# Kernel optimization log

Hardware: AMD Instinct MI355X
Metric: run time of the kernel (lower is better)

Reference implementation:

```python
import jax, jax.numpy as jnp
import numpy as np

BATCH = 4096
DIM = 2048
TEMPERATURE = 0.5


def setup_inputs() -> dict:
    key = jax.random.key(0)
    k1, k2 = jax.random.split(key)
    c_i = jax.random.normal(k1, (BATCH, DIM), dtype=jnp.float32)
    c_j = jax.random.normal(k2, (BATCH, DIM), dtype=jnp.float32)
    return {"c_i": c_i, "c_j": c_j}


def reference(c_i, c_j):
    # Original torch loop computes, for each i,j:
    #   kl[i, j] = sum_k softmax(c_j[j])_k * (log_softmax(c_j[j])_k - log_softmax(c_i[i])_k)
    #   logits = -kl / T ; loss = CE(logits, arange(B), reduction='sum') / B
    # Fused: kl = hneg[None, :] - Li @ Q.T where hneg[j] = sum_k Q[j]*logQ[j].
    B = c_i.shape[0]
    Li = jax.nn.log_softmax(c_i, axis=-1)          # [B, D]
    LQ = jax.nn.log_softmax(c_j, axis=-1)          # [B, D]
    Q = jnp.exp(LQ)                                # softmax(c_j)
    hneg = jnp.sum(Q * LQ, axis=-1)                # [B] negative entropy of each c_j row
    cross = jnp.einsum("id,jd->ij", Li, Q)         # [B, B] sum_k Li[i,k]*Q[j,k]
    kl = hneg[None, :] - cross                     # [B, B]
    logits = -kl / TEMPERATURE
    logp = jax.nn.log_softmax(logits, axis=-1)     # [B, B]
    loss = -jnp.sum(jnp.diagonal(logp)) / B        # CE(sum) / batch_size
    return loss
```

## Files before the change

### kernel.cpp

```cpp
#include <hip/hip_runtime.h>
#include <hip/hip_bf16.h>
#include <math.h>

#define BATCH 4096
#define DIM   2048
#define INV_T 2.0f

#define BM 256
#define BN 256

typedef float floatx4 __attribute__((ext_vector_type(4)));
typedef int   intx4   __attribute__((ext_vector_type(4)));
typedef int   intx8   __attribute__((ext_vector_type(8)));

static __device__ __forceinline__ void gld_lds16(const void* g, void* l) {
  __builtin_amdgcn_global_load_lds(
      (const __attribute__((address_space(1))) void*)g,
      (__attribute__((address_space(3))) void*)l, 16, 0, 0);
}

static __device__ __forceinline__ intx8 comb8(intx4 lo, intx4 hi) {
  intx8 r;
  r[0] = lo[0]; r[1] = lo[1]; r[2] = lo[2]; r[3] = lo[3];
  r[4] = hi[0]; r[5] = hi[1]; r[6] = hi[2]; r[7] = hi[3];
  return r;
}

__global__ __launch_bounds__(256) void prep_kernel(
    const float* __restrict__ ci, const float* __restrict__ cj,
    unsigned char* __restrict__ Li8, unsigned char* __restrict__ Qb8,
    float* __restrict__ hneg, float* __restrict__ isc,
    float* __restrict__ rowsum, float* __restrict__ out)
{
  const int lane = threadIdx.x & 63;
  const int wave = threadIdx.x >> 6;
  const int row = blockIdx.x * 4 + wave;
  const bool isj = row >= BATCH;
  const int r = isj ? row - BATCH : row;
  const float* __restrict__ src = (isj ? cj : ci) + (size_t)r * DIM;

  float v[32];
  #pragma unroll
  for (int i = 0; i < 8; ++i) {
    float4 t = ((const float4*)src)[i * 64 + lane];
    v[i * 4 + 0] = t.x; v[i * 4 + 1] = t.y;
    v[i * 4 + 2] = t.z; v[i * 4 + 3] = t.w;
  }

  float m = v[0];
  #pragma unroll
  for (int i = 1; i < 32; ++i) m = fmaxf(m, v[i]);
  #pragma unroll
  for (int off = 32; off >= 1; off >>= 1) m = fmaxf(m, __shfl_xor(m, off));

  float s = 0.f;
  #pragma unroll
  for (int i = 0; i < 32; ++i) s += __expf(v[i] - m);
  #pragma unroll
  for (int off = 32; off >= 1; off >>= 1) s += __shfl_xor(s, off);
  const float ls = m + __logf(s);

  float scale = 1.f;
  int t = 0;
  if (isj) {
    const float qmax = __expf(m - ls);
    const int be = (int)((__float_as_uint(qmax) >> 23) & 0xff);
    t = 134 - be;
    scale = __uint_as_float((unsigned)(t + 127) << 23);
  }

  unsigned char* dst = (isj ? Qb8 : Li8) + (size_t)r * DIM;
  float h = 0.f;
  #pragma unroll
  for (int i = 0; i < 8; ++i) {
    float f[4];
    #pragma unroll
    for (int j = 0; j < 4; ++j) {
      const float li = v[i * 4 + j] - ls;
      if (isj) {
        const float q = __expf(li);
        h += q * li;
        f[j] = q * scale;
      } else {
        f[j] = li;
      }
    }
    int w = __builtin_amdgcn_cvt_pk_fp8_f32(f[0], f[1], 0, false);
    w = __builtin_amdgcn_cvt_pk_fp8_f32(f[2], f[3], w, true);
    if (isj) {
      const int idx = ((r >> 4) << 13) | ((i * 2 + (lane >> 5)) << 9)
                    | (((lane >> 3) & 3) << 7) | ((r & 15) << 3) | (lane & 7);
      ((int*)Qb8)[idx] = w;
    } else {
      ((int*)dst)[i * 64 + lane] = w;
    }
  }

  if (isj) {
    #pragma unroll
    for (int off = 32; off >= 1; off >>= 1) h += __shfl_xor(h, off);
    if (lane == 0) {
      hneg[r] = h;
      isc[r] = __uint_as_float((unsigned)(127 - t) << 23);
      rowsum[r] = 0.f;
    }
  }
  if (row == 0 && lane == 0) out[0] = 0.f;
}

__global__ __launch_bounds__(512, 1) void gemm_lse_kernel(
    const unsigned char* __restrict__ Li8, const unsigned char* __restrict__ Qb8,
    const float* __restrict__ hneg, const float* __restrict__ isc,
    float* __restrict__ rowsum, float* __restrict__ diag)
{
  __shared__ __attribute__((aligned(16))) unsigned char As_[2][BM * 128];

  const int tid  = threadIdx.x;
  const int lin = blockIdx.x;
  const int xc  = lin & 7;
  const int sq  = lin >> 3;
  const int by  = (xc & 3) * 4 + (sq & 3);
  const int bx  = (xc >> 2) * 8 + (sq >> 2);

  const int lane = tid & 63;
  const int wave = tid >> 6;
  const int wm   = wave >> 2;
  const int wn   = wave & 3;

  int soff[4];
  #pragma unroll
  for (int s = 0; s < 4; ++s) {
    const int p = tid + 512 * s;
    const int row = p >> 3;
    const int cbg = (p & 7) ^ (row & 7);
    soff[s] = row * DIM + cbg * 16;
  }
  const unsigned char* Abase = Li8 + (size_t)(by * BM) * DIM;
  const unsigned char* Bfbase =
      Qb8 + (size_t)(bx * 16 + wn * 4) * 32768 + lane * 32;

  const int rl = lane & 15;
  const int q  = lane >> 4;
  const int sw = rl & 7;

  floatx4 acc[8][4];
  const floatx4 z = {0.f, 0.f, 0.f, 0.f};
  #pragma unroll
  for (int mt = 0; mt < 8; ++mt)
    #pragma unroll
    for (int nt = 0; nt < 4; ++nt) acc[mt][nt] = z;

  #pragma unroll
  for (int s = 0; s < 4; ++s)
    gld_lds16(Abase + soff[s], &As_[0][0] + (tid + 512 * s) * 16);
  intx8 bfA[4], bfB[4];
  #pragma unroll
  for (int nt = 0; nt < 4; ++nt)
    bfA[nt] = comb8(*(const intx4*)(Bfbase + nt * 32768),
                    *(const intx4*)(Bfbase + nt * 32768 + 16));

#define KTILE(T, CUR, bfU, bfN)                                               \
  {                                                                           \
    const int t_ = (T);                                                       \
    const unsigned char* Ab = &As_[CUR][0];                                   \
    if (t_ < 15) {                                                            \
      unsigned char* An = &As_[(CUR) ^ 1][0];                                 \
      const int kn = (t_ + 1) * 128;                                          \
      _Pragma("unroll")                                                       \
      for (int s = 0; s < 4; ++s)                                             \
        gld_lds16(Abase + soff[s] + kn, An + (tid + 512 * s) * 16);           \
      _Pragma("unroll")                                                       \
      for (int nt = 0; nt < 4; ++nt)                                          \
        bfN[nt] = comb8(                                                      \
            *(const intx4*)(Bfbase + nt * 32768 + (t_ + 1) * 2048),           \
            *(const intx4*)(Bfbase + nt * 32768 + (t_ + 1) * 2048 + 16));     \
      asm volatile("s_waitcnt vmcnt(12)" ::: "memory");                       \
    } else {                                                                  \
      asm volatile("s_waitcnt vmcnt(0)" ::: "memory");                        \
    }                                                                         \
    asm volatile("s_barrier" ::: "memory");                                   \
    intx8 af[2];                                                              \
    {                                                                         \
      const int ra = wm * 128 + rl;                                           \
      const int a0 = ra * 8 + ((2 * q) ^ sw);                                 \
      const int a1 = ra * 8 + ((2 * q + 1) ^ sw);                             \
      af[0] = comb8(*(const intx4*)(Ab + a0 * 16),                            \
                    *(const intx4*)(Ab + a1 * 16));                           \
    }                                                                         \
    _Pragma("unroll")                                                         \
    for (int s = 0; s < 8; ++s) {                                             \
      if (s < 7) {                                                            \
        const int ra = wm * 128 + (s + 1) * 16 + rl;                          \
        const int a0 = ra * 8 + ((2 * q) ^ sw);                               \
        const int a1 = ra * 8 + ((2 * q + 1) ^ sw);                           \
        af[(s + 1) & 1] = comb8(*(const intx4*)(Ab + a0 * 16),                \
                                *(const intx4*)(Ab + a1 * 16));               \
      }                                                                       \
      __builtin_amdgcn_s_setprio(1);                                          \
      _Pragma("unroll")                                                       \
      for (int nt = 0; nt < 4; ++nt)                                          \
        acc[s][nt] = __builtin_amdgcn_mfma_scale_f32_16x16x128_f8f6f4(        \
            af[s & 1], bfU[nt], acc[s][nt],                                   \
            0, 0,                     \
            0, 127,                                         \
            0, 127);                                        \
      __builtin_amdgcn_s_setprio(0);                                          \
    }                                                                         \
    asm volatile("s_barrier" ::: "memory");                                   \
  }

  for (int tt = 0; tt < 8; ++tt) {
    KTILE(2 * tt,     0, bfA, bfB);
    KTILE(2 * tt + 1, 1, bfB, bfA);
  }
#undef KTILE

  const int col0 = bx * BN + wn * 64 + rl;
  float hn[4], sc[4];
  #pragma unroll
  for (int nt = 0; nt < 4; ++nt) {
    hn[nt] = hneg[col0 + nt * 16];
    sc[nt] = isc[col0 + nt * 16];
  }
  const int row0 = by * BM + wm * 128 + (q << 2);

  if (bx == by && wm == (wn >> 1) && q == (rl >> 2)) {
    #pragma unroll
    for (int half = 0; half < 2; ++half) {
      #pragma unroll
      for (int nt = 0; nt < 4; ++nt) {
        #pragma unroll
        for (int rr = 0; rr < 4; ++rr) {
          if ((wn & 1) == half && (rl & 3) == rr)
            diag[bx * BN + wn * 64 + nt * 16 + rl] =
                acc[half * 4 + nt][nt][rr] * sc[nt];
        }
      }
    }
  }

  #pragma unroll
  for (int mt = 0; mt < 8; ++mt) {
    #pragma unroll
    for (int rr = 0; rr < 4; ++rr) {
      float p = 0.f;
      #pragma unroll
      for (int nt = 0; nt < 4; ++nt)
        p += __expf(INV_T * (acc[mt][nt][rr] * sc[nt] - hn[nt]));
      p += __shfl_xor(p, 1);
      p += __shfl_xor(p, 2);
      p += __shfl_xor(p, 4);
      p += __shfl_xor(p, 8);
      if (rl == 0)
        atomicAdd(&rowsum[row0 + mt * 16 + rr], p);
    }
  }
}

__global__ __launch_bounds__(256) void finalize_kernel(
    const float* __restrict__ hneg, const float* __restrict__ rowsum,
    const float* __restrict__ diag, float* __restrict__ out)
{
  const int i = blockIdx.x * 256 + threadIdx.x;
  const int lane = threadIdx.x & 63;
  const int wave = threadIdx.x >> 6;

  float c = __logf(rowsum[i]) - INV_T * (diag[i] - hneg[i]);
  #pragma unroll
  for (int off = 32; off >= 1; off >>= 1) c += __shfl_xor(c, off);

  __shared__ float red[4];
  if (lane == 0) red[wave] = c;
  __syncthreads();
  if (threadIdx.x == 0)
    atomicAdd(out, (red[0] + red[1] + red[2] + red[3]) * (1.0f / BATCH));
}

extern "C" void kernel_launch(void* const* d_in, const int* in_sizes, int n_in,
                              void* d_out, int out_size, void* d_ws, size_t ws_size,
                              hipStream_t stream) {
  const float* ci = (const float*)d_in[0];
  const float* cj = (const float*)d_in[1];
  float* out = (float*)d_out;

  unsigned char* Li8 = (unsigned char*)d_ws;
  unsigned char* Qb8 = Li8 + (size_t)BATCH * DIM;
  float* hneg   = (float*)(Qb8 + (size_t)BATCH * DIM);
  float* isc    = hneg + BATCH;
  float* rowsum = isc + BATCH;
  float* diag   = rowsum + BATCH;

  prep_kernel<<<2 * BATCH / 4, 256, 0, stream>>>(ci, cj, Li8, Qb8, hneg, isc, rowsum, out);
  gemm_lse_kernel<<<(BATCH / BM) * (BATCH / BN), 512, 0, stream>>>(Li8, Qb8, hneg, isc, rowsum, diag);
  finalize_kernel<<<BATCH / 256, 256, 0, stream>>>(hneg, rowsum, diag, out);
}
```

Before: 166.6 us.

## Triple-buffer LDS A tiles with single barrier and reuse exp in prep

The GEMM main loop moves from double-buffered to triple-buffered LDS for the A operand. A tiles are prefetched two steps ahead, and each k-tile uses a single barrier instead of two. B fragments no longer ping-pong between two register sets: they are loaded into one set after each tile's MFMAs, which frees registers but may expose B load latency at the start of the next tile. The prep kernel also keeps the exponentials from the sum pass and builds softmax values by multiplying with a reciprocal, which drops a second exp per element.

```diff
diff --git a/kernel.cpp b/kernel.cpp
--- a/kernel.cpp
+++ b/kernel.cpp
@@ -53,23 +53,24 @@
   #pragma unroll
   for (int off = 32; off >= 1; off >>= 1) m = fmaxf(m, __shfl_xor(m, off));
 
+  float e[32];
   float s = 0.f;
   #pragma unroll
-  for (int i = 0; i < 32; ++i) s += __expf(v[i] - m);
+  for (int i = 0; i < 32; ++i) { e[i] = __expf(v[i] - m); s += e[i]; }
   #pragma unroll
   for (int off = 32; off >= 1; off >>= 1) s += __shfl_xor(s, off);
   const float ls = m + __logf(s);
+  const float inv_s = 1.0f / s;
 
   float scale = 1.f;
   int t = 0;
   if (isj) {
-    const float qmax = __expf(m - ls);
-    const int be = (int)((__float_as_uint(qmax) >> 23) & 0xff);
+    const int be = (int)((__float_as_uint(inv_s) >> 23) & 0xff);
     t = 134 - be;
     scale = __uint_as_float((unsigned)(t + 127) << 23);
   }
 
-  unsigned char* dst = (isj ? Qb8 : Li8) + (size_t)r * DIM;
+  unsigned char* dst = Li8 + (size_t)r * DIM;
   float h = 0.f;
   #pragma unroll
   for (int i = 0; i < 8; ++i) {
@@ -78,7 +79,7 @@
     for (int j = 0; j < 4; ++j) {
       const float li = v[i * 4 + j] - ls;
       if (isj) {
-        const float q = __expf(li);
+        const float q = e[i * 4 + j] * inv_s;
         h += q * li;
         f[j] = q * scale;
       } else {
@@ -113,7 +114,7 @@
     const float* __restrict__ hneg, const float* __restrict__ isc,
     float* __restrict__ rowsum, float* __restrict__ diag)
 {
-  __shared__ __attribute__((aligned(16))) unsigned char As_[2][BM * 128];
+  __shared__ __attribute__((aligned(16))) unsigned char As_[3][BM * 128];
 
   const int tid  = threadIdx.x;
   const int lin = blockIdx.x;
@@ -153,32 +154,30 @@
   #pragma unroll
   for (int s = 0; s < 4; ++s)
     gld_lds16(Abase + soff[s], &As_[0][0] + (tid + 512 * s) * 16);
-  intx8 bfA[4], bfB[4];
+  #pragma unroll
+  for (int s = 0; s < 4; ++s)
+    gld_lds16(Abase + soff[s] + 128, &As_[1][0] + (tid + 512 * s) * 16);
+  intx8 bf[4];
   #pragma unroll
   for (int nt = 0; nt < 4; ++nt)
-    bfA[nt] = comb8(*(const intx4*)(Bfbase + nt * 32768),
-                    *(const intx4*)(Bfbase + nt * 32768 + 16));
-
-#define KTILE(T, CUR, bfU, bfN)                                               \
+    bf[nt] = comb8(*(const intx4*)(Bfbase + nt * 32768),
+                   *(const intx4*)(Bfbase + nt * 32768 + 16));
+
+#define KTILE(T, CURBUF, STGBUF)                                              \
   {                                                                           \
     const int t_ = (T);                                                       \
-    const unsigned char* Ab = &As_[CUR][0];                                   \
-    if (t_ < 15) {                                                            \
-      unsigned char* An = &As_[(CUR) ^ 1][0];                                 \
-      const int kn = (t_ + 1) * 128;                                          \
+    asm volatile("s_barrier" ::: "memory");                                   \
+    if (t_ <= 13) {                                                           \
+      const int kn = (t_ + 2) * 128;                                          \
       _Pragma("unroll")                                                       \
       for (int s = 0; s < 4; ++s)                                             \
-        gld_lds16(Abase + soff[s] + kn, An + (tid + 512 * s) * 16);           \
-      _Pragma("unroll")                                                       \
-      for (int nt = 0; nt < 4; ++nt)                                          \
-        bfN[nt] = comb8(                                                      \
-            *(const intx4*)(Bfbase + nt * 32768 + (t_ + 1) * 2048),           \
-            *(const intx4*)(Bfbase + nt * 32768 + (t_ + 1) * 2048 + 16));     \
-      asm volatile("s_waitcnt vmcnt(12)" ::: "memory");                       \
+        gld_lds16(Abase + soff[s] + kn,                                       \
+                  &As_[STGBUF][0] + (tid + 512 * s) * 16);                    \
+      asm volatile("s_waitcnt vmcnt(4)" ::: "memory");                        \
     } else {                                                                  \
       asm volatile("s_waitcnt vmcnt(0)" ::: "memory");                        \
     }                                                                         \
-    asm volatile("s_barrier" ::: "memory");                                   \
+    const unsigned char* Ab = &As_[CURBUF][0];                                \
     intx8 af[2];                                                              \
     {                                                                         \
       const int ra = wm * 128 + rl;                                           \
@@ -200,19 +199,28 @@
       _Pragma("unroll")                                                       \
       for (int nt = 0; nt < 4; ++nt)                                          \
         acc[s][nt] = __builtin_amdgcn_mfma_scale_f32_16x16x128_f8f6f4(        \
-            af[s & 1], bfU[nt], acc[s][nt],                                   \
+            af[s & 1], bf[nt], acc[s][nt],                                    \
             0, 0,                     \
             0, 127,                                         \
             0, 127);                                        \
       __builtin_amdgcn_s_setprio(0);                                          \
     }                                                                         \
-    asm volatile("s_barrier" ::: "memory");                                   \
-  }
-
-  for (int tt = 0; tt < 8; ++tt) {
-    KTILE(2 * tt,     0, bfA, bfB);
-    KTILE(2 * tt + 1, 1, bfB, bfA);
-  }
+    if (t_ <= 14) {                                                           \
+        \
+      const unsigned char* Bt = Bfbase + (t_ + 1) * 2048;                     \
+      _Pragma("unroll")                                                       \
+      for (int nt = 0; nt < 4; ++nt)                                          \
+        bf[nt] = comb8(*(const intx4*)(Bt + nt * 32768),                      \
+                       *(const intx4*)(Bt + nt * 32768 + 16));                \
+    }                                                                         \
+  }
+
+  for (int tt = 0; tt < 5; ++tt) {
+    KTILE(3 * tt + 0, 0, 2);
+    KTILE(3 * tt + 1, 1, 0);
+    KTILE(3 * tt + 2, 2, 1);
+  }
+  KTILE(15, 0, 2);
 #undef KTILE
 
   const int col0 = bx * BN + wn * 64 + rl;
```

Measured after the change: 161.5 us. 1.03x faster.
